# Performance work log

Hardware: AMD Instinct MI355X
Metric: run time of the kernel (lower is better)

## Reference

```python
import jax, jax.numpy as jnp
import numpy as np

B, S, D, F, R = 4, 2048, 2048, 8192, 16


def setup_inputs() -> dict:
    key = jax.random.key(0)
    ks = jax.random.split(key, 13)
    sc = 0.02  # weight scale to keep activations well-conditioned
    return {
        "x1": jax.random.normal(ks[0], (B, S, D), jnp.float32),
        "w_gate": jax.random.normal(ks[1], (D, F), jnp.float32) * sc,
        "b_gate": jax.random.normal(ks[2], (F,), jnp.float32) * sc,
        "w_gate_lora_a": jax.random.normal(ks[3], (D, R), jnp.float32) * sc,
        "w_gate_lora_b": jax.random.normal(ks[4], (R, F), jnp.float32) * sc,
        "w_up": jax.random.normal(ks[5], (D, F), jnp.float32) * sc,
        "b_up": jax.random.normal(ks[6], (F,), jnp.float32) * sc,
        "w_up_lora_a": jax.random.normal(ks[7], (D, R), jnp.float32) * sc,
        "w_up_lora_b": jax.random.normal(ks[8], (R, F), jnp.float32) * sc,
        "w_down": jax.random.normal(ks[9], (F, D), jnp.float32) * sc,
        "b_down": jax.random.normal(ks[10], (D,), jnp.float32) * sc,
        "w_down_lora_a": jax.random.normal(ks[11], (F, R), jnp.float32) * sc,
        "w_down_lora_b": jax.random.normal(ks[12], (R, D), jnp.float32) * sc,
    }


def reference(x1, w_gate, b_gate, w_gate_lora_a, w_gate_lora_b,
              w_up, b_up, w_up_lora_a, w_up_lora_b,
              w_down, b_down, w_down_lora_a, w_down_lora_b):
    # gate projection: dequantized base GEMM + bias + rank-R LoRA
    y1 = x1 @ w_gate + b_gate + (x1 @ w_gate_lora_a) @ w_gate_lora_b  # [B,S,F]
    # up projection
    y2 = x1 @ w_up + b_up + (x1 @ w_up_lora_a) @ w_up_lora_b          # [B,S,F]
    # activation_forward == 'relu' gated product
    x3 = jax.nn.relu(y1) * y2                                          # [B,S,F]
    # down projection
    y3 = x3 @ w_down + b_down + (x3 @ w_down_lora_a) @ w_down_lora_b  # [B,S,D]
    return y3
```

## Files before the change

kernel.cpp:

```cpp
#include <hip/hip_runtime.h>

typedef __bf16 bf16x8 __attribute__((ext_vector_type(8)));
typedef float f32x4 __attribute__((ext_vector_type(4)));

#define MFMA16(a, b, c) __builtin_amdgcn_mfma_f32_16x16x32_bf16((a), (b), (c), 0, 0, 0)

__device__ __forceinline__ unsigned short f2bf(float f) {
    unsigned int u = __float_as_uint(f);
    u += 0x7fffu + ((u >> 16) & 1u);
    return (unsigned short)(u >> 16);
}

__device__ __forceinline__ void gload16(const unsigned short* g, unsigned short* l) {
    __builtin_amdgcn_global_load_lds(
        (__attribute__((address_space(1))) void*)(void*)g,
        (__attribute__((address_space(3))) void*)(void*)l,
        16, 0, 0);
}


__global__ void cast_x_kernel(const float4* __restrict__ x, ushort4* __restrict__ xb) {
    const size_t i = (size_t)blockIdx.x * 256 + threadIdx.x;
    const float4 v = x[i];
    ushort4 o;
    o.x = f2bf(v.x); o.y = f2bf(v.y); o.z = f2bf(v.z); o.w = f2bf(v.w);
    xb[i] = o;
}

__global__ void prep_wT(const float* __restrict__ W, const float* __restrict__ A,
                        const float* __restrict__ B2, unsigned short* __restrict__ WT,
                        const int K, const int N) {
    __shared__ float tile[64][65];
    __shared__ float As[64][16];
    __shared__ float Bs[16][64];
    const int t = threadIdx.x;
    const int k0 = blockIdx.x * 64;
    const int n0 = blockIdx.y * 64;

    for (int i = t; i < 64 * 16; i += 256)
        As[i >> 4][i & 15] = A[(size_t)(k0 + (i >> 4)) * 16 + (i & 15)];
    for (int i = t; i < 16 * 64; i += 256)
        Bs[i >> 6][i & 63] = B2[(size_t)(i >> 6) * N + n0 + (i & 63)];
    __syncthreads();

    const int c = t & 63;
    const int r0 = t >> 6;
    for (int rr = 0; rr < 64; rr += 4) {
        const int r = rr + r0;
        float v = W[(size_t)(k0 + r) * N + n0 + c];
#pragma unroll
        for (int q = 0; q < 16; ++q) v += As[r][q] * Bs[q][c];
        tile[r][c] = v;
    }
    __syncthreads();
    for (int rr = 0; rr < 64; rr += 4) {
        const int r = rr + r0;
        WT[(size_t)(n0 + r) * K + k0 + c] = f2bf(tile[c][r]);
    }
}

__global__ __launch_bounds__(256, 2)
void gemm_gateup(const unsigned short* __restrict__ Xb,
                 const unsigned short* __restrict__ WgT,
                 const unsigned short* __restrict__ WuT,
                 const float* __restrict__ bg, const float* __restrict__ bu,
                 unsigned short* __restrict__ X3) {
    constexpr int K = 2048, F = 8192;
    constexpr int BK = 64;
    __shared__ __align__(16) unsigned short As[128 * BK];
    __shared__ __align__(16) unsigned short Bg[128 * BK];
    __shared__ __align__(16) unsigned short Bu[128 * BK];

    const int tid = threadIdx.x;
    const int lane = tid & 63;
    const int wave = tid >> 6;
    const int wm = (wave >> 1) * 64;
    const int wn = (wave & 1) * 64;
    const int l16 = lane & 15;
    const int quad = lane >> 4;

    const int m0 = blockIdx.x * 128;
    const int n0 = blockIdx.y * 128;

    const unsigned short* Ag = Xb + (size_t)m0 * K;
    const unsigned short* Gg = WgT + (size_t)n0 * K;
    const unsigned short* Ug = WuT + (size_t)n0 * K;

    int srow[4], soff[4];
#pragma unroll
    for (int j = 0; j < 4; ++j) {
        const int c = tid + j * 256;
        srow[j] = c >> 3;
        soff[j] = ((c & 7) ^ (srow[j] & 7)) * 8;
    }

    f32x4 accg[4][4] = {};
    f32x4 accu[4][4] = {};

    for (int k0 = 0; k0 < K; k0 += BK) {
#pragma unroll
        for (int j = 0; j < 4; ++j)
            gload16(Ag + (size_t)srow[j] * K + k0 + soff[j], As + (tid + j * 256) * 8);
#pragma unroll
        for (int j = 0; j < 4; ++j)
            gload16(Gg + (size_t)srow[j] * K + k0 + soff[j], Bg + (tid + j * 256) * 8);
#pragma unroll
        for (int j = 0; j < 4; ++j)
            gload16(Ug + (size_t)srow[j] * K + k0 + soff[j], Bu + (tid + j * 256) * 8);
        __syncthreads();
#pragma unroll
        for (int h = 0; h < 2; ++h) {
            bf16x8 af[4], gf[4], uf[4];
#pragma unroll
            for (int i = 0; i < 4; ++i) {
                const int ra = wm + i * 16 + l16;
                const int rb = wn + i * 16 + l16;
                const int pa = ((h * 4 + quad) ^ (ra & 7)) * 8;
                const int pb = ((h * 4 + quad) ^ (rb & 7)) * 8;
                af[i] = *(const bf16x8*)(As + ra * BK + pa);
                gf[i] = *(const bf16x8*)(Bg + rb * BK + pb);
                uf[i] = *(const bf16x8*)(Bu + rb * BK + pb);
            }
#pragma unroll
            for (int i = 0; i < 4; ++i)
#pragma unroll
                for (int j = 0; j < 4; ++j) {
                    accg[i][j] = MFMA16(af[i], gf[j], accg[i][j]);
                    accu[i][j] = MFMA16(af[i], uf[j], accu[i][j]);
                }
        }
        __syncthreads();
    }

#pragma unroll
    for (int j = 0; j < 4; ++j) {
        const int col = n0 + wn + j * 16 + l16;
        const float bgv = bg[col];
        const float buv = bu[col];
#pragma unroll
        for (int i = 0; i < 4; ++i) {
            const int rowb = m0 + wm + i * 16 + quad * 4;
#pragma unroll
            for (int r = 0; r < 4; ++r) {
                float g = accg[i][j][r] + bgv;
                float u = accu[i][j][r] + buv;
                g = g > 0.f ? g : 0.f;
                X3[(size_t)(rowb + r) * F + col] = f2bf(g * u);
            }
        }
    }
}

__global__ __launch_bounds__(256, 3)
void gemm_down(const unsigned short* __restrict__ X3,
               const unsigned short* __restrict__ WdT,
               const float* __restrict__ bd, float* __restrict__ out) {
    constexpr int K = 8192, N = 2048;
    constexpr int BK = 64;
    __shared__ __align__(16) unsigned short As[128 * BK];
    __shared__ __align__(16) unsigned short Bs[128 * BK];

    const int tid = threadIdx.x;
    const int lane = tid & 63;
    const int wave = tid >> 6;
    const int wm = (wave >> 1) * 64;
    const int wn = (wave & 1) * 64;
    const int l16 = lane & 15;
    const int quad = lane >> 4;

    const int m0 = blockIdx.x * 128;
    const int n0 = blockIdx.y * 128;

    const unsigned short* Ag = X3 + (size_t)m0 * K;
    const unsigned short* Bgp = WdT + (size_t)n0 * K;

    int srow[4], soff[4];
#pragma unroll
    for (int j = 0; j < 4; ++j) {
        const int c = tid + j * 256;
        srow[j] = c >> 3;
        soff[j] = ((c & 7) ^ (srow[j] & 7)) * 8;
    }

    f32x4 acc[4][4] = {};

    for (int k0 = 0; k0 < K; k0 += BK) {
#pragma unroll
        for (int j = 0; j < 4; ++j)
            gload16(Ag + (size_t)srow[j] * K + k0 + soff[j], As + (tid + j * 256) * 8);
#pragma unroll
        for (int j = 0; j < 4; ++j)
            gload16(Bgp + (size_t)srow[j] * K + k0 + soff[j], Bs + (tid + j * 256) * 8);
        __syncthreads();
#pragma unroll
        for (int h = 0; h < 2; ++h) {
            bf16x8 af[4], bfr[4];
#pragma unroll
            for (int i = 0; i < 4; ++i) {
                const int ra = wm + i * 16 + l16;
                const int rb = wn + i * 16 + l16;
                const int pa = ((h * 4 + quad) ^ (ra & 7)) * 8;
                const int pb = ((h * 4 + quad) ^ (rb & 7)) * 8;
                af[i] = *(const bf16x8*)(As + ra * BK + pa);
                bfr[i] = *(const bf16x8*)(Bs + rb * BK + pb);
            }
#pragma unroll
            for (int i = 0; i < 4; ++i)
#pragma unroll
                for (int j = 0; j < 4; ++j)
                    acc[i][j] = MFMA16(af[i], bfr[j], acc[i][j]);
        }
        __syncthreads();
    }

#pragma unroll
    for (int j = 0; j < 4; ++j) {
        const int col = n0 + wn + j * 16 + l16;
        const float bdv = bd[col];
#pragma unroll
        for (int i = 0; i < 4; ++i) {
            const int rowb = m0 + wm + i * 16 + quad * 4;
#pragma unroll
            for (int r = 0; r < 4; ++r)
                out[(size_t)(rowb + r) * N + col] = acc[i][j][r] + bdv;
        }
    }
}

extern "C" void kernel_launch(void* const* d_in, const int* in_sizes, int n_in,
                              void* d_out, int out_size, void* d_ws, size_t ws_size,
                              hipStream_t stream) {
    const float* x1      = (const float*)d_in[0];
    const float* w_gate  = (const float*)d_in[1];
    const float* b_gate  = (const float*)d_in[2];
    const float* a_gate  = (const float*)d_in[3];
    const float* lb_gate = (const float*)d_in[4];
    const float* w_up    = (const float*)d_in[5];
    const float* b_up    = (const float*)d_in[6];
    const float* a_up    = (const float*)d_in[7];
    const float* lb_up   = (const float*)d_in[8];
    const float* w_down  = (const float*)d_in[9];
    const float* b_down  = (const float*)d_in[10];
    const float* a_down  = (const float*)d_in[11];
    const float* lb_down = (const float*)d_in[12];

    constexpr int M = 8192, D = 2048, F = 8192;

    char* ws = (char*)d_ws;
    unsigned short* Xb  = (unsigned short*)ws;
    unsigned short* WgT = (unsigned short*)(ws + 33554432ULL);
    unsigned short* WuT = (unsigned short*)(ws + 67108864ULL);
    unsigned short* WdT = (unsigned short*)(ws + 100663296ULL);
    unsigned short* X3  = (unsigned short*)(ws + 134217728ULL);

    cast_x_kernel<<<dim3((M * D) / 4 / 256), dim3(256), 0, stream>>>(
        (const float4*)x1, (ushort4*)Xb);
    prep_wT<<<dim3(D / 64, F / 64), dim3(256), 0, stream>>>(w_gate, a_gate, lb_gate, WgT, D, F);
    prep_wT<<<dim3(D / 64, F / 64), dim3(256), 0, stream>>>(w_up, a_up, lb_up, WuT, D, F);
    prep_wT<<<dim3(F / 64, D / 64), dim3(256), 0, stream>>>(w_down, a_down, lb_down, WdT, F, D);

    gemm_gateup<<<dim3(M / 128, F / 128), dim3(256), 0, stream>>>(
        Xb, WgT, WuT, b_gate, b_up, X3);
    gemm_down<<<dim3(M / 128, D / 128), dim3(256), 0, stream>>>(
        X3, WdT, b_down, (float*)d_out);
}
```

Measured before the change: 1.112 ms.

## Double-buffer gate/up GEMM with 512-thread 256x128 tiles and interleaved prefetch

```diff
diff --git a/kernel.cpp b/kernel.cpp
--- a/kernel.cpp
+++ b/kernel.cpp
@@ -18,6 +18,28 @@
         16, 0, 0);
 }
 
+
+__device__ __forceinline__ void ld_frag4(const unsigned short* base, int w0, int h,
+                                         int l16, int quad, bf16x8* f) {
+#pragma unroll
+    for (int i = 0; i < 4; ++i) {
+        const int r = w0 + i * 16 + l16;
+        f[i] = *(const bf16x8*)(base + r * 64 + (((h * 4 + quad) ^ (r & 7)) * 8));
+    }
+}
+
+__device__ __forceinline__ void mfma16x(const bf16x8* af, const bf16x8* bf, f32x4 (*acc)[4]) {
+    __builtin_amdgcn_s_setprio(1);
+#pragma unroll
+    for (int i = 0; i < 4; ++i)
+#pragma unroll
+        for (int j = 0; j < 4; ++j) acc[i][j] = MFMA16(af[i], bf[j], acc[i][j]);
+    __builtin_amdgcn_s_setprio(0);
+}
+
+#define ASM_VMCNT2 asm volatile("s_waitcnt vmcnt(2)" ::: "memory")
+#define ASM_VMCNT0 asm volatile("s_waitcnt vmcnt(0)" ::: "memory")
+#define ASM_LGKM0  asm volatile("s_waitcnt lgkmcnt(0)" ::: "memory")
 
 __global__ void cast_x_kernel(const float4* __restrict__ x, ushort4* __restrict__ xb) {
     const size_t i = (size_t)blockIdx.x * 256 + threadIdx.x;
@@ -59,17 +81,17 @@
     }
 }
 
-__global__ __launch_bounds__(256, 2)
+__global__ __launch_bounds__(512, 2)
 void gemm_gateup(const unsigned short* __restrict__ Xb,
                  const unsigned short* __restrict__ WgT,
                  const unsigned short* __restrict__ WuT,
                  const float* __restrict__ bg, const float* __restrict__ bu,
                  unsigned short* __restrict__ X3) {
-    constexpr int K = 2048, F = 8192;
-    constexpr int BK = 64;
-    __shared__ __align__(16) unsigned short As[128 * BK];
-    __shared__ __align__(16) unsigned short Bg[128 * BK];
-    __shared__ __align__(16) unsigned short Bu[128 * BK];
+    constexpr int K = 2048, F = 8192, BK = 64, NT = K / BK;
+    extern __shared__ __align__(16) unsigned short lds[];
+    unsigned short* const A0 = lds;
+    unsigned short* const G0 = lds + 32768;
+    unsigned short* const U0 = lds + 49152;
 
     const int tid = threadIdx.x;
     const int lane = tid & 63;
@@ -79,58 +101,94 @@
     const int l16 = lane & 15;
     const int quad = lane >> 4;
 
-    const int m0 = blockIdx.x * 128;
+    const int m0 = blockIdx.x * 256;
     const int n0 = blockIdx.y * 128;
 
     const unsigned short* Ag = Xb + (size_t)m0 * K;
     const unsigned short* Gg = WgT + (size_t)n0 * K;
     const unsigned short* Ug = WuT + (size_t)n0 * K;
 
-    int srow[4], soff[4];
-#pragma unroll
-    for (int j = 0; j < 4; ++j) {
-        const int c = tid + j * 256;
+    int srow[2], soff[2];
+#pragma unroll
+    for (int j = 0; j < 2; ++j) {
+        const int c = tid + j * 512;
         srow[j] = c >> 3;
         soff[j] = ((c & 7) ^ (srow[j] & 7)) * 8;
     }
+    const int dst0 = tid * 8, dst1 = (tid + 512) * 8;
+
+#define STAGE(gptr, lbase, kk, roff)                                                        \
+    do {                                                                                    \
+        gload16((gptr) + (size_t)(srow[0] + (roff)) * K + (kk) + soff[0], (lbase) + dst0);  \
+        gload16((gptr) + (size_t)(srow[1] + (roff)) * K + (kk) + soff[1], (lbase) + dst1);  \
+    } while (0)
 
     f32x4 accg[4][4] = {};
     f32x4 accu[4][4] = {};
-
-    for (int k0 = 0; k0 < K; k0 += BK) {
-#pragma unroll
-        for (int j = 0; j < 4; ++j)
-            gload16(Ag + (size_t)srow[j] * K + k0 + soff[j], As + (tid + j * 256) * 8);
-#pragma unroll
-        for (int j = 0; j < 4; ++j)
-            gload16(Gg + (size_t)srow[j] * K + k0 + soff[j], Bg + (tid + j * 256) * 8);
-#pragma unroll
-        for (int j = 0; j < 4; ++j)
-            gload16(Ug + (size_t)srow[j] * K + k0 + soff[j], Bu + (tid + j * 256) * 8);
-        __syncthreads();
-#pragma unroll
-        for (int h = 0; h < 2; ++h) {
-            bf16x8 af[4], gf[4], uf[4];
-#pragma unroll
-            for (int i = 0; i < 4; ++i) {
-                const int ra = wm + i * 16 + l16;
-                const int rb = wn + i * 16 + l16;
-                const int pa = ((h * 4 + quad) ^ (ra & 7)) * 8;
-                const int pb = ((h * 4 + quad) ^ (rb & 7)) * 8;
-                af[i] = *(const bf16x8*)(As + ra * BK + pa);
-                gf[i] = *(const bf16x8*)(Bg + rb * BK + pb);
-                uf[i] = *(const bf16x8*)(Bu + rb * BK + pb);
-            }
-#pragma unroll
-            for (int i = 0; i < 4; ++i)
-#pragma unroll
-                for (int j = 0; j < 4; ++j) {
-                    accg[i][j] = MFMA16(af[i], gf[j], accg[i][j]);
-                    accu[i][j] = MFMA16(af[i], uf[j], accu[i][j]);
-                }
+    bf16x8 af[4], bfr[4];
+
+    STAGE(Ag, A0, 0, 0);
+    STAGE(Ag, A0 + 8192, 0, 128);
+    STAGE(Gg, G0, 0, 0);
+    STAGE(Ug, U0, 0, 0);
+    ASM_VMCNT2;
+    __builtin_amdgcn_s_barrier();
+    __builtin_amdgcn_sched_barrier(0);
+
+    for (int t = 0; t < NT; ++t) {
+        const int p = t & 1, q = p ^ 1;
+        const unsigned short* Ap = A0 + p * 16384;
+        const unsigned short* Gp = G0 + p * 8192;
+        const unsigned short* Up = U0 + p * 8192;
+        unsigned short* const Aq = A0 + q * 16384;
+        unsigned short* const Gq = G0 + q * 8192;
+        unsigned short* const Uq = U0 + q * 8192;
+        const int kn = (t + 1) * BK;
+        const bool pf = (t + 1 < NT);
+
+        ld_frag4(Ap, wm, 0, l16, quad, af);
+        ld_frag4(Gp, wn, 0, l16, quad, bfr);
+        if (pf) STAGE(Ag, Aq, kn, 0);
+        __builtin_amdgcn_s_barrier();
+        ASM_LGKM0;
+        __builtin_amdgcn_sched_barrier(0);
+        mfma16x(af, bfr, accg);
+        if (pf) {
+            ASM_VMCNT2;
+        } else {
+            ASM_VMCNT0;
         }
-        __syncthreads();
-    }
+        __builtin_amdgcn_s_barrier();
+        __builtin_amdgcn_sched_barrier(0);
+
+        ld_frag4(Up, wn, 0, l16, quad, bfr);
+        if (pf) STAGE(Ag, Aq + 8192, kn, 128);
+        __builtin_amdgcn_s_barrier();
+        ASM_LGKM0;
+        __builtin_amdgcn_sched_barrier(0);
+        mfma16x(af, bfr, accu);
+        __builtin_amdgcn_s_barrier();
+
+        ld_frag4(Ap, wm, 1, l16, quad, af);
+        ld_frag4(Gp, wn, 1, l16, quad, bfr);
+        if (pf) STAGE(Gg, Gq, kn, 0);
+        __builtin_amdgcn_s_barrier();
+        ASM_LGKM0;
+        __builtin_amdgcn_sched_barrier(0);
+        mfma16x(af, bfr, accg);
+        __builtin_amdgcn_s_barrier();
+
+        ld_frag4(Up, wn, 1, l16, quad, bfr);
+        if (pf) STAGE(Ug, Uq, kn, 0);
+        __builtin_amdgcn_s_barrier();
+        ASM_LGKM0;
+        __builtin_amdgcn_sched_barrier(0);
+        mfma16x(af, bfr, accu);
+        ASM_VMCNT2;
+        __builtin_amdgcn_s_barrier();
+        __builtin_amdgcn_sched_barrier(0);
+    }
+#undef STAGE
 
 #pragma unroll
     for (int j = 0; j < 4; ++j) {
@@ -246,6 +304,13 @@
 
     constexpr int M = 8192, D = 2048, F = 8192;
 
+    static bool attr_set = false;
+    if (!attr_set) {
+        (void)hipFuncSetAttribute((const void*)gemm_gateup,
+                                  hipFuncAttributeMaxDynamicSharedMemorySize, 131072);
+        attr_set = true;
+    }
+
     char* ws = (char*)d_ws;
     unsigned short* Xb  = (unsigned short*)ws;
     unsigned short* WgT = (unsigned short*)(ws + 33554432ULL);
@@ -259,7 +324,7 @@
     prep_wT<<<dim3(D / 64, F / 64), dim3(256), 0, stream>>>(w_up, a_up, lb_up, WuT, D, F);
     prep_wT<<<dim3(F / 64, D / 64), dim3(256), 0, stream>>>(w_down, a_down, lb_down, WdT, F, D);
 
-    gemm_gateup<<<dim3(M / 128, F / 128), dim3(256), 0, stream>>>(
+    gemm_gateup<<<dim3(M / 256, F / 128), dim3(512), 131072, stream>>>(
         Xb, WgT, WuT, b_gate, b_up, X3);
     gemm_down<<<dim3(M / 128, D / 128), dim3(256), 0, stream>>>(
         X3, WdT, b_down, (float*)d_out);
```

Result: faster. 1.049 ms (-5.7%).
